# Kernel optimization log

Measured on AMD Instinct MI355X. Metric: run time of the kernel, lower is better.

## Reference

```python
import jax, jax.numpy as jnp
import numpy as np

HID = 2048
HEADS = 16
HD = HID // HEADS  # 128
EPS = 1e-6


def setup_inputs() -> dict:
    key = jax.random.key(0)
    ks = jax.random.split(key, 9)
    s = 1.0 / np.sqrt(HID)
    return {
        "hidden_states": jax.random.normal(ks[0], (4, 4096, HID), jnp.float32),
        "q_w": jax.random.normal(ks[1], (HID, HID), jnp.float32) * s,
        "q_b": jnp.zeros((HID,), jnp.float32),
        "k_w": jax.random.normal(ks[2], (HID, HID), jnp.float32) * s,
        "k_b": jnp.zeros((HID,), jnp.float32),
        "v_w": jax.random.normal(ks[3], (HID, HID), jnp.float32) * s,
        "v_b": jnp.zeros((HID,), jnp.float32),
        "o_w": jax.random.normal(ks[4], (HID, HID), jnp.float32) * s,
        "o_b": jnp.zeros((HID,), jnp.float32),
    }


def _heads(x, b, s):
    # [B,S,HID] -> [B,H,S,Dh]
    return x.reshape(b, s, HEADS, HD).transpose(0, 2, 1, 3)


def reference(hidden_states, q_w, q_b, k_w, k_b, v_w, v_b, o_w, o_b):
    b, s, _ = hidden_states.shape
    # torch Linear: y = x @ W.T + b
    q = _heads(hidden_states @ q_w.T + q_b, b, s)
    k = _heads(hidden_states @ k_w.T + k_b, b, s)
    v = _heads(hidden_states @ v_w.T + v_b, b, s)
    # kernel feature map: elu(x) + 1
    qp = jax.nn.elu(q) + 1.0
    kp = jax.nn.elu(k) + 1.0
    # KV outer-product reduction over sequence: [B,H,Dh,Dh]
    kv = jnp.einsum('bhsd,bhse->bhde', kp, v)
    # normalizer z = q' @ sum_s k'  -> [B,H,S,1]
    z = jnp.einsum('bhsd,bhd->bhs', qp, kp.sum(axis=2))[..., None]
    attn = jnp.einsum('bhsd,bhde->bhse', qp, kv) / (z + EPS)
    out = attn.transpose(0, 2, 1, 3).reshape(b, s, HID)
    return out @ o_w.T + o_b
```

## Files before the change

kernel.cpp:

```cpp
#include <hip/hip_runtime.h>
#include <hip/hip_bf16.h>

#define HIDC 2048
#define NHEADS 16
#define HDIM 128
#define NB 4
#define NS 4096
#define NROWS (NB*NS)
#define QSTR 6144
#define EPSV 1e-6f

typedef __attribute__((ext_vector_type(8))) short s16x8;
typedef __attribute__((ext_vector_type(4))) float f32x4;
typedef __attribute__((ext_vector_type(8))) unsigned short u16x8;

static __device__ __forceinline__ unsigned short f2b(float f) {
  unsigned int u = __float_as_uint(f);
  u += 0x7fffu + ((u >> 16) & 1u);
  return (unsigned short)(u >> 16);
}
static __device__ __forceinline__ float b2f(unsigned short h) {
  return __uint_as_float(((unsigned int)h) << 16);
}

static __device__ __forceinline__ void gload_lds16(const unsigned short* g, unsigned short* l) {
  __builtin_amdgcn_global_load_lds(
      (const __attribute__((address_space(1))) void*)g,
      (__attribute__((address_space(3))) void*)l, 16, 0, 0);
}

__global__ __launch_bounds__(256) void convert_all(
    const float* __restrict__ hs, const float* __restrict__ qw,
    const float* __restrict__ kw, const float* __restrict__ vw,
    const float* __restrict__ ow,
    unsigned short* __restrict__ hsb, unsigned short* __restrict__ qwb,
    unsigned short* __restrict__ kwb, unsigned short* __restrict__ vwb,
    unsigned short* __restrict__ owb)
{
  int bid = blockIdx.x;
  const float* src; unsigned short* dst; size_t base;
  if (bid < 16384) { src = hs; dst = hsb; base = (size_t)bid << 11; }
  else {
    int t = bid - 16384; int wsel = t >> 11; int wb = t & 2047;
    src = wsel == 0 ? qw : wsel == 1 ? kw : wsel == 2 ? vw : ow;
    dst = wsel == 0 ? qwb : wsel == 1 ? kwb : wsel == 2 ? vwb : owb;
    base = (size_t)wb << 11;
  }
  size_t i = base + ((size_t)threadIdx.x << 3);
  float4 a = *(const float4*)(src + i);
  float4 b = *(const float4*)(src + i + 4);
  u16x8 o;
  o[0] = f2b(a.x); o[1] = f2b(a.y); o[2] = f2b(a.z); o[3] = f2b(a.w);
  o[4] = f2b(b.x); o[5] = f2b(b.y); o[6] = f2b(b.z); o[7] = f2b(b.w);
  *(u16x8*)(dst + i) = o;
}

template<int QKV, int OUT_BF16>
__global__ __launch_bounds__(512, 2) void gemm256(
    const unsigned short* __restrict__ A,
    const unsigned short* __restrict__ B0,
    const unsigned short* __restrict__ B1,
    const unsigned short* __restrict__ B2,
    const float* __restrict__ bias0,
    const float* __restrict__ bias1,
    const float* __restrict__ bias2,
    void* __restrict__ Cp,
    int mtile, int astr, int ostr)
{
  __shared__ unsigned short lds[65536];
  const int tid = threadIdx.x;
  const int lane = tid & 63, wid = tid >> 6;
  const int wr = wid >> 2, wc = wid & 3;
  const int l15 = lane & 15, l4 = lane >> 4;

  const int cpx = (int)gridDim.x >> 3;
  const int bidx = (int)blockIdx.x;
  const int wg = (bidx & 7) * cpx + (bidx >> 3);
  const int bm = (wg % mtile) << 8;
  const int bn = (wg / mtile) << 8;

  const unsigned short* Bp = B0;
  const float* bias = bias0;
  bool act = false;
  int bnw = bn;
  if (QKV) {
    int seg = bn >> 11;
    Bp = seg == 0 ? B0 : (seg == 1 ? B1 : B2);
    bias = seg == 0 ? bias0 : (seg == 1 ? bias1 : bias2);
    act = seg < 2;
    bnw = bn & 2047;
  }

  const int c0 = wid << 1;
  const int srow = lane >> 2;
  const int scol = (((lane & 3) ^ ((srow >> 1) & 3)) << 3);
  const unsigned short* Asrc0 = A + (size_t)(bm + (c0 << 4) + srow) * astr + scol;
  const unsigned short* Asrc1 = Asrc0 + (size_t)16 * astr;
  const unsigned short* Bsrc0 = Bp + (size_t)(bnw + (c0 << 4) + srow) * HIDC + scol;
  const unsigned short* Bsrc1 = Bsrc0 + (size_t)16 * HIDC;
  const int adst = c0 << 9;

  const int xa = ((l4 ^ ((l15 >> 1) & 3)) << 3);
  const int abase = ((wr << 7) + l15) * 32 + xa;
  const int bbase = 8192 + ((wc << 6) + l15) * 32 + xa;

  f32x4 acc[8][4] = {};

#define STAGE_A(s_) { const int sl_ = ((s_) & 3) << 14; const int kt_ = (s_) << 5; \
    gload_lds16(Asrc0 + kt_, &lds[sl_ + adst]); \
    gload_lds16(Asrc1 + kt_, &lds[sl_ + adst + 512]); }
#define STAGE_B(s_) { const int sl_ = ((s_) & 3) << 14; const int kt_ = (s_) << 5; \
    gload_lds16(Bsrc0 + kt_, &lds[sl_ + 8192 + adst]); \
    gload_lds16(Bsrc1 + kt_, &lds[sl_ + 8192 + adst + 512]); }

#define DO_STEP(s_, STG, GATE) { \
    const int sl = ((s_) & 3) << 14; \
    s16x8 a[8], bl[2], bh[2]; \
    _Pragma("unroll") for (int mf = 0; mf < 8; ++mf) \
      a[mf] = *(const s16x8*)&lds[sl + abase + (mf << 9)]; \
    bl[0] = *(const s16x8*)&lds[sl + bbase]; \
    bl[1] = *(const s16x8*)&lds[sl + bbase + 512]; \
    if (STG) STAGE_A((s_) + 3); \
    __builtin_amdgcn_s_barrier(); \
    __builtin_amdgcn_s_setprio(1); \
    _Pragma("unroll") for (int mf = 0; mf < 8; ++mf) { \
      acc[mf][0] = __builtin_amdgcn_mfma_f32_16x16x32_bf16(a[mf], bl[0], acc[mf][0], 0, 0, 0); \
      acc[mf][1] = __builtin_amdgcn_mfma_f32_16x16x32_bf16(a[mf], bl[1], acc[mf][1], 0, 0, 0); } \
    __builtin_amdgcn_s_setprio(0); \
    __builtin_amdgcn_s_barrier(); \
    bh[0] = *(const s16x8*)&lds[sl + bbase + 1024]; \
    bh[1] = *(const s16x8*)&lds[sl + bbase + 1536]; \
    if (STG) STAGE_B((s_) + 3); \
    __builtin_amdgcn_s_barrier(); \
    __builtin_amdgcn_s_setprio(1); \
    _Pragma("unroll") for (int mf = 0; mf < 8; ++mf) { \
      acc[mf][2] = __builtin_amdgcn_mfma_f32_16x16x32_bf16(a[mf], bh[0], acc[mf][2], 0, 0, 0); \
      acc[mf][3] = __builtin_amdgcn_mfma_f32_16x16x32_bf16(a[mf], bh[1], acc[mf][3], 0, 0, 0); } \
    __builtin_amdgcn_s_setprio(0); \
    if ((GATE) == 8)      { asm volatile("s_waitcnt vmcnt(8)" ::: "memory"); } \
    else if ((GATE) == 4) { asm volatile("s_waitcnt vmcnt(4)" ::: "memory"); } \
    else if ((GATE) == 0) { asm volatile("s_waitcnt vmcnt(0)" ::: "memory"); } \
    __builtin_amdgcn_s_barrier(); \
    __builtin_amdgcn_sched_barrier(0); \
  }

  STAGE_A(0); STAGE_B(0);
  STAGE_A(1); STAGE_B(1);
  STAGE_A(2); STAGE_B(2);
  asm volatile("s_waitcnt vmcnt(8)" ::: "memory");
  __builtin_amdgcn_s_barrier();
  __builtin_amdgcn_sched_barrier(0);

  for (int s = 0; s < 61; ++s) DO_STEP(s, 1, 8);
  DO_STEP(61, 0, 4);
  DO_STEP(62, 0, 0);
  DO_STEP(63, 0, -1);

#undef DO_STEP
#undef STAGE_A
#undef STAGE_B

  #pragma unroll
  for (int nf = 0; nf < 4; ++nf) {
    const int colw = (wc << 6) + (nf << 4) + l15;
    const float bv = bias[bnw + colw];
    #pragma unroll
    for (int mf = 0; mf < 8; ++mf) {
      #pragma unroll
      for (int r = 0; r < 4; ++r) {
        const int row = bm + (wr << 7) + (mf << 4) + (l4 << 2) + r;
        float v = acc[mf][nf][r] + bv;
        if (QKV) { if (act) v = (v > 0.f) ? (v + 1.f) : __expf(v); }
        const size_t off = (size_t)row * ostr + bn + colw;
        if (OUT_BF16) ((unsigned short*)Cp)[off] = f2b(v);
        else          ((float*)Cp)[off] = v;
      }
    }
  }
}

__global__ __launch_bounds__(256) void kv_partial(
    const unsigned short* __restrict__ kp, const unsigned short* __restrict__ vv,
    float* __restrict__ kvp, float* __restrict__ ksp)
{
  const int bh = blockIdx.x >> 3;
  const int chunk = blockIdx.x & 7;
  const int b = bh >> 4, h = bh & 15;
  const int tid = threadIdx.x;
  const int td = tid >> 4, te = tid & 15;

  __shared__ float kpl[32][128];
  __shared__ float vl[32][132];

  float acc[8][8] = {};
  float ks[8] = {};

  const size_t rowbase = (size_t)b * NS * QSTR + (size_t)h * HDIM;
  const int s0 = chunk * 512;

  for (int st = 0; st < 512; st += 32) {
    __syncthreads();
    #pragma unroll
    for (int i = 0; i < 2; ++i) {
      int idx = tid + (i << 8);
      int row = idx >> 4, q = idx & 15;
      size_t g = rowbase + (size_t)(s0 + st + row) * QSTR + (q << 3);
      u16x8 k8 = *(const u16x8*)(kp + g);
      u16x8 v8 = *(const u16x8*)(vv + g);
      float tk[8], tv[8];
      #pragma unroll
      for (int j = 0; j < 8; ++j) { tk[j] = b2f(k8[j]); tv[j] = b2f(v8[j]); }
      *(float4*)&kpl[row][(q << 3)]     = make_float4(tk[0], tk[1], tk[2], tk[3]);
      *(float4*)&kpl[row][(q << 3) + 4] = make_float4(tk[4], tk[5], tk[6], tk[7]);
      *(float4*)&vl[row][(q << 3)]      = make_float4(tv[0], tv[1], tv[2], tv[3]);
      *(float4*)&vl[row][(q << 3) + 4]  = make_float4(tv[4], tv[5], tv[6], tv[7]);
    }
    __syncthreads();
    #pragma unroll 4
    for (int s = 0; s < 32; ++s) {
      float kd[8], ve[8];
      *(float4*)&kd[0] = *(const float4*)&kpl[s][td << 3];
      *(float4*)&kd[4] = *(const float4*)&kpl[s][(td << 3) + 4];
      *(float4*)&ve[0] = *(const float4*)&vl[s][te << 3];
      *(float4*)&ve[4] = *(const float4*)&vl[s][(te << 3) + 4];
      if (te == 0) {
        #pragma unroll
        for (int i = 0; i < 8; ++i) ks[i] += kd[i];
      }
      #pragma unroll
      for (int i = 0; i < 8; ++i)
        #pragma unroll
        for (int j = 0; j < 8; ++j)
          acc[i][j] += kd[i] * ve[j];
    }
  }

  float* outp = kvp + ((size_t)(chunk * 64 + bh) << 14);
  #pragma unroll
  for (int j = 0; j < 8; ++j) {
    int e = (te << 3) + j;
    float r0[8];
    #pragma unroll
    for (int i = 0; i < 8; ++i) r0[i] = acc[i][j];
    *(float4*)&outp[(size_t)e * HDIM + (td << 3)]     = *(float4*)&r0[0];
    *(float4*)&outp[(size_t)e * HDIM + (td << 3) + 4] = *(float4*)&r0[4];
  }
  if (te == 0) {
    float* kso = ksp + ((size_t)(chunk * 64 + bh) << 7) + (td << 3);
    #pragma unroll
    for (int i = 0; i < 8; ++i) kso[i] = ks[i];
  }
}

__global__ __launch_bounds__(256) void kv_reduce(
    const float* __restrict__ kvp, float* __restrict__ kvT)
{
  int i = blockIdx.x * 256 + threadIdx.x;
  float s = 0.f;
  #pragma unroll
  for (int c = 0; c < 8; ++c) s += kvp[(size_t)c * (64 * 16384) + i];
  kvT[i] = s;
}

__global__ __launch_bounds__(256) void attn_ker(
    const unsigned short* __restrict__ qp, const float* __restrict__ kvT,
    const float* __restrict__ ksp, unsigned short* __restrict__ attn)
{
  const int bh = blockIdx.x >> 5, stile = blockIdx.x & 31;
  const int b = bh >> 4, h = bh & 15;
  const int tid = threadIdx.x;
  const int lane = tid & 63, w = tid >> 6;
  const int l15 = lane & 15, l4 = lane >> 4;

  __shared__ unsigned short Qs[128][136];
  __shared__ unsigned short Ks[128][136];
  __shared__ float ksl[128];
  __shared__ float zs[128];

  const size_t qbase = ((size_t)b * NS + (size_t)stile * 128) * QSTR + (size_t)h * HDIM;

  #pragma unroll
  for (int i = 0; i < 8; ++i) {
    int idx = tid + (i << 8);
    int row = idx >> 4, q = idx & 15;
    u16x8 v8 = *(const u16x8*)(qp + qbase + (size_t)row * QSTR + (q << 3));
    *(u16x8*)&Qs[row][q << 3] = v8;
  }
  const float* kvb = kvT + ((size_t)bh << 14);
  #pragma unroll
  for (int i = 0; i < 16; ++i) {
    int idx = tid + (i << 8);
    int row = idx >> 5, q = idx & 31;
    float4 v4 = *(const float4*)(kvb + (size_t)row * HDIM + (q << 2));
    ushort4 w4; w4.x = f2b(v4.x); w4.y = f2b(v4.y); w4.z = f2b(v4.z); w4.w = f2b(v4.w);
    *(ushort4*)&Ks[row][q << 2] = w4;
  }
  if (tid < 128) {
    float s = 0.f;
    #pragma unroll
    for (int c = 0; c < 8; ++c) s += ksp[((size_t)(c * 64 + bh) << 7) + tid];
    ksl[tid] = s;
  }
  __syncthreads();
  if (tid < 128) {
    float z = 0.f;
    #pragma unroll
    for (int dq = 0; dq < 16; ++dq) {
      u16x8 qv = *(const u16x8*)&Qs[tid][dq << 3];
      #pragma unroll
      for (int j = 0; j < 8; ++j) z += b2f(qv[j]) * ksl[(dq << 3) + j];
    }
    zs[tid] = 1.f / (z + EPSV);
  }
  __syncthreads();

  f32x4 acc[2][8] = {};
  #pragma unroll
  for (int kk = 0; kk < 4; ++kk) {
    s16x8 a[2], bb[8];
    #pragma unroll
    for (int mf = 0; mf < 2; ++mf)
      a[mf] = *(const s16x8*)&Qs[(w << 5) + (mf << 4) + l15][(kk << 5) + (l4 << 3)];
    #pragma unroll
    for (int nf = 0; nf < 8; ++nf)
      bb[nf] = *(const s16x8*)&Ks[(nf << 4) + l15][(kk << 5) + (l4 << 3)];
    #pragma unroll
    for (int mf = 0; mf < 2; ++mf)
      #pragma unroll
      for (int nf = 0; nf < 8; ++nf)
        acc[mf][nf] = __builtin_amdgcn_mfma_f32_16x16x32_bf16(a[mf], bb[nf], acc[mf][nf], 0, 0, 0);
  }

  #pragma unroll
  for (int mf = 0; mf < 2; ++mf) {
    #pragma unroll
    for (int r = 0; r < 4; ++r) {
      const int rl = (w << 5) + (mf << 4) + (l4 << 2) + r;
      const float zi = zs[rl];
      #pragma unroll
      for (int nf = 0; nf < 8; ++nf) {
        const int e = (nf << 4) + l15;
        attn[qbase + (size_t)rl * QSTR + e] = f2b(acc[mf][nf][r] * zi);
      }
    }
  }
}

extern "C" void kernel_launch(void* const* d_in, const int* in_sizes, int n_in,
                              void* d_out, int out_size, void* d_ws, size_t ws_size,
                              hipStream_t stream) {
  const float* hs = (const float*)d_in[0];
  const float* qw = (const float*)d_in[1];
  const float* qb = (const float*)d_in[2];
  const float* kw = (const float*)d_in[3];
  const float* kb = (const float*)d_in[4];
  const float* vw = (const float*)d_in[5];
  const float* vb = (const float*)d_in[6];
  const float* ow = (const float*)d_in[7];
  const float* ob = (const float*)d_in[8];

  char* w = (char*)d_ws;
  unsigned short* hsb = (unsigned short*)(w);
  unsigned short* qwb = (unsigned short*)(w + 67108864);
  unsigned short* kwb = (unsigned short*)(w + 75497472);
  unsigned short* vwb = (unsigned short*)(w + 83886080);
  unsigned short* owb = (unsigned short*)(w + 92274688);
  unsigned short* qkv = (unsigned short*)(w + 100663296);
  float* kvp = (float*)(w);
  float* ksp = (float*)(w + 33554432);
  float* kvT = (float*)(w + 33816576);

  convert_all<<<dim3(24576), dim3(256), 0, stream>>>(hs, qw, kw, vw, ow, hsb, qwb, kwb, vwb, owb);
  gemm256<1, 1><<<dim3(24 * 64), dim3(512), 0, stream>>>(
      hsb, qwb, kwb, vwb, qb, kb, vb, qkv, 64, HIDC, QSTR);
  kv_partial<<<dim3(512), dim3(256), 0, stream>>>(qkv + 2048, qkv + 4096, kvp, ksp);
  kv_reduce<<<dim3(4096), dim3(256), 0, stream>>>(kvp, kvT);
  attn_ker<<<dim3(2048), dim3(256), 0, stream>>>(qkv, kvT, ksp, qkv + 4096);
  gemm256<0, 0><<<dim3(8 * 64), dim3(512), 0, stream>>>(
      qkv + 4096, owb, owb, owb, ob, ob, ob, d_out, 64, QSTR, HIDC);
}
```

Baseline: 830.7 us.

## Group GEMM tiles by M-chunks and restructure MFMA step to load all B fragments first

```diff
diff --git a/kernel.cpp b/kernel.cpp
--- a/kernel.cpp
+++ b/kernel.cpp
@@ -65,7 +65,7 @@
     const float* __restrict__ bias1,
     const float* __restrict__ bias2,
     void* __restrict__ Cp,
-    int mtile, int astr, int ostr)
+    int ntile, int astr, int ostr)
 {
   __shared__ unsigned short lds[65536];
   const int tid = threadIdx.x;
@@ -76,8 +76,11 @@
   const int cpx = (int)gridDim.x >> 3;
   const int bidx = (int)blockIdx.x;
   const int wg = (bidx & 7) * cpx + (bidx >> 3);
-  const int bm = (wg % mtile) << 8;
-  const int bn = (wg / mtile) << 8;
+  const int csz = ntile << 2;
+  const int chunk = wg / csz;
+  const int t = wg % csz;
+  const int bm = ((chunk << 2) + (t & 3)) << 8;
+  const int bn = (t >> 2) << 8;
 
   const unsigned short* Bp = B0;
   const float* bias = bias0;
@@ -113,35 +116,45 @@
     gload_lds16(Bsrc0 + kt_, &lds[sl_ + 8192 + adst]); \
     gload_lds16(Bsrc1 + kt_, &lds[sl_ + 8192 + adst + 512]); }
 
+#define MM4(ai_, r_) { \
+    acc[r_][0] = __builtin_amdgcn_mfma_f32_16x16x32_bf16(ai_, b0, acc[r_][0], 0, 0, 0); \
+    acc[r_][1] = __builtin_amdgcn_mfma_f32_16x16x32_bf16(ai_, b1, acc[r_][1], 0, 0, 0); \
+    acc[r_][2] = __builtin_amdgcn_mfma_f32_16x16x32_bf16(ai_, b2, acc[r_][2], 0, 0, 0); \
+    acc[r_][3] = __builtin_amdgcn_mfma_f32_16x16x32_bf16(ai_, b3, acc[r_][3], 0, 0, 0); }
+
 #define DO_STEP(s_, STG, GATE) { \
     const int sl = ((s_) & 3) << 14; \
-    s16x8 a[8], bl[2], bh[2]; \
-    _Pragma("unroll") for (int mf = 0; mf < 8; ++mf) \
-      a[mf] = *(const s16x8*)&lds[sl + abase + (mf << 9)]; \
-    bl[0] = *(const s16x8*)&lds[sl + bbase]; \
-    bl[1] = *(const s16x8*)&lds[sl + bbase + 512]; \
+     \
+    s16x8 b0 = *(const s16x8*)&lds[sl + bbase]; \
+    s16x8 b1 = *(const s16x8*)&lds[sl + bbase + 512]; \
+    s16x8 b2 = *(const s16x8*)&lds[sl + bbase + 1024]; \
+    s16x8 b3 = *(const s16x8*)&lds[sl + bbase + 1536]; \
+    s16x8 a0 = *(const s16x8*)&lds[sl + abase]; \
+    s16x8 a1 = *(const s16x8*)&lds[sl + abase + 512]; \
+    s16x8 a2 = *(const s16x8*)&lds[sl + abase + 1024]; \
+    s16x8 a3 = *(const s16x8*)&lds[sl + abase + 1536]; \
     if (STG) STAGE_A((s_) + 3); \
     __builtin_amdgcn_s_barrier(); \
+    asm volatile("s_waitcnt lgkmcnt(0)" ::: "memory"); \
     __builtin_amdgcn_s_setprio(1); \
-    _Pragma("unroll") for (int mf = 0; mf < 8; ++mf) { \
-      acc[mf][0] = __builtin_amdgcn_mfma_f32_16x16x32_bf16(a[mf], bl[0], acc[mf][0], 0, 0, 0); \
-      acc[mf][1] = __builtin_amdgcn_mfma_f32_16x16x32_bf16(a[mf], bl[1], acc[mf][1], 0, 0, 0); } \
+    MM4(a0, 0) MM4(a1, 1) MM4(a2, 2) MM4(a3, 3) \
     __builtin_amdgcn_s_setprio(0); \
     __builtin_amdgcn_s_barrier(); \
-    bh[0] = *(const s16x8*)&lds[sl + bbase + 1024]; \
-    bh[1] = *(const s16x8*)&lds[sl + bbase + 1536]; \
+     \
+    s16x8 a4 = *(const s16x8*)&lds[sl + abase + 2048]; \
+    s16x8 a5 = *(const s16x8*)&lds[sl + abase + 2560]; \
+    s16x8 a6 = *(const s16x8*)&lds[sl + abase + 3072]; \
+    s16x8 a7 = *(const s16x8*)&lds[sl + abase + 3584]; \
     if (STG) STAGE_B((s_) + 3); \
     __builtin_amdgcn_s_barrier(); \
+    asm volatile("s_waitcnt lgkmcnt(0)" ::: "memory"); \
     __builtin_amdgcn_s_setprio(1); \
-    _Pragma("unroll") for (int mf = 0; mf < 8; ++mf) { \
-      acc[mf][2] = __builtin_amdgcn_mfma_f32_16x16x32_bf16(a[mf], bh[0], acc[mf][2], 0, 0, 0); \
-      acc[mf][3] = __builtin_amdgcn_mfma_f32_16x16x32_bf16(a[mf], bh[1], acc[mf][3], 0, 0, 0); } \
+    MM4(a4, 4) MM4(a5, 5) MM4(a6, 6) MM4(a7, 7) \
     __builtin_amdgcn_s_setprio(0); \
     if ((GATE) == 8)      { asm volatile("s_waitcnt vmcnt(8)" ::: "memory"); } \
     else if ((GATE) == 4) { asm volatile("s_waitcnt vmcnt(4)" ::: "memory"); } \
     else if ((GATE) == 0) { asm volatile("s_waitcnt vmcnt(0)" ::: "memory"); } \
     __builtin_amdgcn_s_barrier(); \
-    __builtin_amdgcn_sched_barrier(0); \
   }
 
   STAGE_A(0); STAGE_B(0);
@@ -149,7 +162,6 @@
   STAGE_A(2); STAGE_B(2);
   asm volatile("s_waitcnt vmcnt(8)" ::: "memory");
   __builtin_amdgcn_s_barrier();
-  __builtin_amdgcn_sched_barrier(0);
 
   for (int s = 0; s < 61; ++s) DO_STEP(s, 1, 8);
   DO_STEP(61, 0, 4);
@@ -157,6 +169,7 @@
   DO_STEP(63, 0, -1);
 
 #undef DO_STEP
+#undef MM4
 #undef STAGE_A
 #undef STAGE_B
 
@@ -372,10 +385,10 @@
 
   convert_all<<<dim3(24576), dim3(256), 0, stream>>>(hs, qw, kw, vw, ow, hsb, qwb, kwb, vwb, owb);
   gemm256<1, 1><<<dim3(24 * 64), dim3(512), 0, stream>>>(
-      hsb, qwb, kwb, vwb, qb, kb, vb, qkv, 64, HIDC, QSTR);
+      hsb, qwb, kwb, vwb, qb, kb, vb, qkv, 24, HIDC, QSTR);
   kv_partial<<<dim3(512), dim3(256), 0, stream>>>(qkv + 2048, qkv + 4096, kvp, ksp);
   kv_reduce<<<dim3(4096), dim3(256), 0, stream>>>(kvp, kvT);
   attn_ker<<<dim3(2048), dim3(256), 0, stream>>>(qkv, kvT, ksp, qkv + 4096);
   gemm256<0, 0><<<dim3(8 * 64), dim3(512), 0, stream>>>(
-      qkv + 4096, owb, owb, owb, ob, ob, ob, d_out, 64, QSTR, HIDC);
-}
+      qkv + 4096, owb, owb, owb, ob, ob, ob, d_out, 8, QSTR, HIDC);
+}
```

New measurement: 783.8 us. 1.06x faster.
